# Kernel tuning notes

Hardware: AMD Instinct MI355X
Metric: run time of the kernel (lower is better)

Reference implementation:

```python
import jax, jax.numpy as jnp
import numpy as np

N = 50000      # nodes
E = 800000     # graph edges
NNZ = 800000   # hypergraph incidence entries
M = 10000      # hyperedges
IN, HID, OUT = 128, 64, 64


def setup_inputs() -> dict:
    key = jax.random.key(0)
    ks = jax.random.split(key, 12)
    x = jax.random.normal(ks[0], (N, IN), dtype=jnp.float32)
    edge_index = jax.random.randint(ks[1], (2, E), 0, N)
    node_idx = jax.random.randint(ks[2], (NNZ,), 0, N)
    he_idx = jax.random.randint(ks[3], (NNZ,), 0, M)
    hyperedge_index = jnp.stack([node_idx, he_idx])
    w = lambda k, fi, fo: jax.random.normal(k, (fi, fo), jnp.float32) / np.sqrt(fi)
    return {
        "x": x,
        "edge_index": edge_index,
        "hyperedge_index": hyperedge_index,
        "gcn1_w": w(ks[4], IN, HID), "gcn1_b": jnp.zeros((HID,), jnp.float32),
        "gcn2_w": w(ks[5], HID, OUT), "gcn2_b": jnp.zeros((OUT,), jnp.float32),
        "hyper1_w": w(ks[6], IN, HID), "hyper1_b": jnp.zeros((HID,), jnp.float32),
        "hyper2_w": w(ks[7], HID, OUT), "hyper2_b": jnp.zeros((OUT,), jnp.float32),
        "fusion_gate": jnp.zeros((1,), jnp.float32),
    }


def gcn_conv(x, edge_index, w, b):
    # PyG GCNConv: add self-loops, symmetric normalization, then aggregate.
    xw = x @ w
    loops = jnp.arange(N)
    row = jnp.concatenate([edge_index[0], loops])  # source j
    col = jnp.concatenate([edge_index[1], loops])  # target i
    deg = jax.ops.segment_sum(jnp.ones_like(col, dtype=xw.dtype), col, num_segments=N)
    dis = jnp.where(deg > 0, jax.lax.rsqrt(jnp.maximum(deg, 1e-12)), 0.0)
    norm = dis[row] * dis[col]
    out = jax.ops.segment_sum(norm[:, None] * xw[row], col, num_segments=N)
    return out + b


def hyper_conv(x, hyperedge_index, w, b):
    # PyG HypergraphConv (no attention, unit hyperedge weights):
    # out = D^{-1} H B^{-1} H^T (X W) + b
    xw = x @ w
    node_idx, he_idx = hyperedge_index[0], hyperedge_index[1]
    ones = jnp.ones((hyperedge_index.shape[1],), dtype=xw.dtype)
    D = jax.ops.segment_sum(ones, node_idx, num_segments=N)   # node degree
    B = jax.ops.segment_sum(ones, he_idx, num_segments=M)     # hyperedge degree
    Dinv = jnp.where(D > 0, 1.0 / jnp.maximum(D, 1e-12), 0.0)
    Binv = jnp.where(B > 0, 1.0 / jnp.maximum(B, 1e-12), 0.0)
    edge_feat = Binv[:, None] * jax.ops.segment_sum(xw[node_idx], he_idx, num_segments=M)
    out = Dinv[:, None] * jax.ops.segment_sum(edge_feat[he_idx], node_idx, num_segments=N)
    return out + b


def reference(x, edge_index, hyperedge_index,
              gcn1_w, gcn1_b, gcn2_w, gcn2_b,
              hyper1_w, hyper1_b, hyper2_w, hyper2_b,
              fusion_gate):
    # dropout is identity in eval mode (deterministic reference)
    x_s = gcn_conv(x, edge_index, gcn1_w, gcn1_b)
    x_s = jax.nn.elu(x_s)
    x_s = gcn_conv(x_s, edge_index, gcn2_w, gcn2_b)
    x_d = hyper_conv(x, hyperedge_index, hyper1_w, hyper1_b)
    x_d = jax.nn.elu(x_d)
    x_d = hyper_conv(x_d, hyperedge_index, hyper2_w, hyper2_b)
    alpha = jax.nn.sigmoid(fusion_gate)  # shape (1,), broadcasts
    z = alpha * x_s + (1.0 - alpha) * x_d
    return (z, x_s, x_d)
```

## Files before the change

kernel.cpp:

```cpp
#include <hip/hip_runtime.h>
#include <hip/hip_bf16.h>

#define N_NODES 50000
#define N_EDGES 800000
#define NNZ_H   800000
#define M_HE    10000
#define F_IN    128
#define F_HID   64

#define SH_E 7
#define NB_E ((N_NODES + 127) >> 7)
#define SH_H 5
#define NB_H ((M_HE + 31) >> 5)
#define SH_N 7
#define NB_N ((N_NODES + 127) >> 7)
#define TILE 4096
#define GB   ((N_EDGES + TILE - 1) / TILE)
#define NBMAX 400
#define KPBMAX 128
#define GG  782
#define GWN 12500

static __device__ __forceinline__ float bflo(unsigned v) { return __uint_as_float(v << 16); }
static __device__ __forceinline__ float bfhi(unsigned v) { return __uint_as_float(v & 0xFFFF0000u); }

__global__ void k_hist_all(const int* __restrict__ e_col, const int* __restrict__ h_idx,
                           const int* __restrict__ n_idx,
                           int* __restrict__ bcntE, int* __restrict__ bcntH, int* __restrict__ bcntN) {
    __shared__ int hE[NB_E], hH[NB_H], hN[NB_N];
    for (int i = threadIdx.x; i < NB_E; i += 256) hE[i] = 0;
    for (int i = threadIdx.x; i < NB_H; i += 256) hH[i] = 0;
    for (int i = threadIdx.x; i < NB_N; i += 256) hN[i] = 0;
    __syncthreads();
    int stride = gridDim.x * 256;
    for (int i = blockIdx.x * 256 + threadIdx.x; i < N_EDGES; i += stride) {
        atomicAdd(&hE[e_col[i] >> SH_E], 1);
        atomicAdd(&hH[h_idx[i] >> SH_H], 1);
        atomicAdd(&hN[n_idx[i] >> SH_N], 1);
    }
    __syncthreads();
    for (int i = threadIdx.x; i < NB_E; i += 256) if (hE[i]) atomicAdd(&bcntE[i], hE[i]);
    for (int i = threadIdx.x; i < NB_H; i += 256) if (hH[i]) atomicAdd(&bcntH[i], hH[i]);
    for (int i = threadIdx.x; i < NB_N; i += 256) if (hN[i]) atomicAdd(&bcntN[i], hN[i]);
}

__device__ void scan_block(const int* __restrict__ in, int* __restrict__ out, int n) {
    __shared__ int s[1024];
    int t = threadIdx.x;
    int chunk = (n + 1023) >> 10;
    int b = t * chunk;
    int e = min(b + chunk, n);
    int sum = 0;
    for (int i = b; i < e; ++i) sum += in[i];
    s[t] = sum;
    __syncthreads();
    for (int d = 1; d < 1024; d <<= 1) {
        int v = (t >= d) ? s[t - d] : 0;
        __syncthreads();
        s[t] += v;
        __syncthreads();
    }
    int run = (t > 0) ? s[t - 1] : 0;
    for (int i = b; i < e; ++i) { int v = in[i]; out[i] = run; run += v; }
}
__global__ void k_scan_buckets(const int* __restrict__ bcntE, int* __restrict__ boffE,
                               const int* __restrict__ bcntH, int* __restrict__ boffH,
                               const int* __restrict__ bcntN, int* __restrict__ boffN) {
    if (blockIdx.x == 0)      scan_block(bcntE, boffE, NB_E);
    else if (blockIdx.x == 1) scan_block(bcntH, boffH, NB_H);
    else                      scan_block(bcntN, boffN, NB_N);
}

__device__ void chunk_scatter(const int* __restrict__ keys, const int* __restrict__ vals,
                              int n, int sh, int nb,
                              const int* __restrict__ boff, int* __restrict__ bcur,
                              int* __restrict__ bk, int blk) {
    __shared__ int h[NBMAX], loc[NBMAX], base[NBMAX], hc[NBMAX];
    __shared__ int buf[TILE];
    __shared__ unsigned short bkt[TILE];
    int t0 = blk * TILE;
    int tend = min(t0 + TILE, n);
    int cnt = tend - t0;
    for (int b = threadIdx.x; b < nb; b += 256) { h[b] = 0; hc[b] = 0; }
    __syncthreads();
    for (int i = t0 + threadIdx.x; i < tend; i += 256)
        atomicAdd(&h[keys[i] >> sh], 1);
    __syncthreads();
    if (threadIdx.x == 0) {
        int run = 0;
        for (int b = 0; b < nb; ++b) { loc[b] = run; run += h[b]; }
    }
    __syncthreads();
    for (int b = threadIdx.x; b < nb; b += 256)
        base[b] = boff[b] + atomicAdd(&bcur[b], h[b]);
    __syncthreads();
    for (int i = t0 + threadIdx.x; i < tend; i += 256) {
        int k = keys[i];
        int b = k >> sh;
        int r = loc[b] + atomicAdd(&hc[b], 1);
        buf[r] = ((k - (b << sh)) << 16) | vals[i];
        bkt[r] = (unsigned short)b;
    }
    __syncthreads();
    for (int j = threadIdx.x; j < cnt; j += 256) {
        int b = bkt[j];
        bk[base[b] + (j - loc[b])] = buf[j];
    }
}
__global__ void k_chunk_all(const int* __restrict__ e_row, const int* __restrict__ e_col,
                            const int* __restrict__ n_idx, const int* __restrict__ h_idx,
                            const int* __restrict__ boffE, int* __restrict__ bcurE, int* __restrict__ bkE,
                            const int* __restrict__ boffH, int* __restrict__ bcurH, int* __restrict__ bkH,
                            const int* __restrict__ boffN, int* __restrict__ bcurN, int* __restrict__ bkN) {
    int gb = blockIdx.x;
    if (gb < GB)            chunk_scatter(e_col, e_row, N_EDGES, SH_E, NB_E, boffE, bcurE, bkE, gb);
    else if (gb < 2 * GB)   chunk_scatter(h_idx, n_idx, NNZ_H,  SH_H, NB_H, boffH, bcurH, bkH, gb - GB);
    else                    chunk_scatter(n_idx, h_idx, NNZ_H,  SH_N, NB_N, boffN, bcurN, bkN, gb - 2 * GB);
}

__global__ void k_fin_all(const int* __restrict__ bkE, const int* __restrict__ boffE,
                          int* __restrict__ srtE, int* __restrict__ offE,
                          const int* __restrict__ bkH, const int* __restrict__ boffH,
                          int* __restrict__ srtH, int* __restrict__ offH,
                          const int* __restrict__ bkN, const int* __restrict__ boffN,
                          int* __restrict__ srtN, int* __restrict__ offN) {
    __shared__ int koff[KPBMAX];
    __shared__ int kcur[KPBMAX];
    __shared__ int tsum[256];
    int b = blockIdx.x;
    const int* bk; const int* boff; int* srt; int* off;
    int nb, sh, nkeys, total;
    if (b < NB_E) {
        bk = bkE; boff = boffE; srt = srtE; off = offE;
        nb = NB_E; sh = SH_E; nkeys = N_NODES; total = N_EDGES;
    } else if (b < NB_E + NB_H) {
        b -= NB_E;
        bk = bkH; boff = boffH; srt = srtH; off = offH;
        nb = NB_H; sh = SH_H; nkeys = M_HE; total = NNZ_H;
    } else {
        b -= NB_E + NB_H;
        bk = bkN; boff = boffN; srt = srtN; off = offN;
        nb = NB_N; sh = SH_N; nkeys = N_NODES; total = NNZ_H;
    }
    int kpb = 1 << sh;
    int k0 = b << sh;
    int beg = boff[b];
    int end = (b + 1 < nb) ? boff[b + 1] : total;
    int t = threadIdx.x;
    if (t < kpb) { koff[t] = 0; kcur[t] = 0; }
    __syncthreads();
    for (int i = beg + t; i < end; i += 256)
        atomicAdd(&koff[((unsigned)bk[i]) >> 16], 1);
    __syncthreads();
    int v = (t < kpb) ? koff[t] : 0;
    tsum[t] = v;
    __syncthreads();
    for (int d = 1; d < 256; d <<= 1) {
        int u = (t >= d) ? tsum[t - d] : 0;
        __syncthreads();
        tsum[t] += u;
        __syncthreads();
    }
    if (t < kpb) koff[t] = tsum[t] - v;
    __syncthreads();
    if (t < kpb && (k0 + t) < nkeys) off[k0 + t] = beg + koff[t];
    if (b == nb - 1 && t == 0) off[nkeys] = total;
    for (int i = beg + t; i < end; i += 256) {
        int p = bk[i];
        int lk = ((unsigned)p) >> 16;
        int pos = beg + koff[lk] + atomicAdd(&kcur[lk], 1);
        srt[pos] = p & 0xFFFF;
    }
}

template<int K, bool SCALE>
__device__ __forceinline__ void gemm_body(const float* __restrict__ xin, const float* __restrict__ w,
                                          const int* __restrict__ offE, __hip_bfloat16* __restrict__ out,
                                          int blk, float* __restrict__ wl, float* __restrict__ xs) {
    int tid = threadIdx.x;
    int wv = tid >> 6, lane = tid & 63;
    int cg = lane & 15;
    int rg = lane >> 4;
    int rl = wv * 16 + rg * 4;
    int r0 = blk * 64;
    float acc[4][4] = {};
    for (int k0 = 0; k0 < K; k0 += 64) {
        {
            const float4* wsrc = (const float4*)(w + k0 * 64);
            float4* wdst = (float4*)wl;
            for (int j = tid; j < 1024; j += 256) wdst[j] = wsrc[j];
        }
        for (int p = tid; p < 1024; p += 256) {
            int r = p >> 4, c4 = p & 15;
            int row = min(r0 + r, N_NODES - 1);
            float4 vv = *(const float4*)(xin + (size_t)row * K + k0 + 4 * c4);
            *(float4*)&xs[r * 68 + 4 * c4] = vv;
        }
        __syncthreads();
#pragma unroll 4
        for (int kk = 0; kk < 64; ++kk) {
            float4 wf = *(const float4*)&wl[kk * 64 + cg * 4];
            float x0 = xs[(rl + 0) * 68 + kk];
            float x1 = xs[(rl + 1) * 68 + kk];
            float x2 = xs[(rl + 2) * 68 + kk];
            float x3 = xs[(rl + 3) * 68 + kk];
            acc[0][0] += x0 * wf.x; acc[0][1] += x0 * wf.y; acc[0][2] += x0 * wf.z; acc[0][3] += x0 * wf.w;
            acc[1][0] += x1 * wf.x; acc[1][1] += x1 * wf.y; acc[1][2] += x1 * wf.z; acc[1][3] += x1 * wf.w;
            acc[2][0] += x2 * wf.x; acc[2][1] += x2 * wf.y; acc[2][2] += x2 * wf.z; acc[2][3] += x2 * wf.w;
            acc[3][0] += x3 * wf.x; acc[3][1] += x3 * wf.y; acc[3][2] += x3 * wf.z; acc[3][3] += x3 * wf.w;
        }
        __syncthreads();
    }
#pragma unroll
    for (int i = 0; i < 4; ++i) {
        int row = r0 + rl + i;
        if (row < N_NODES) {
            float s = 1.0f;
            if (SCALE) {
                float deg = (float)(offE[row + 1] - offE[row]);
                s = rsqrtf(deg + 1.0f);
            }
            __hip_bfloat16 hv[4];
            hv[0] = __float2bfloat16(acc[i][0] * s);
            hv[1] = __float2bfloat16(acc[i][1] * s);
            hv[2] = __float2bfloat16(acc[i][2] * s);
            hv[3] = __float2bfloat16(acc[i][3] * s);
            *(ushort4*)&out[(size_t)row * 64 + cg * 4] = *(ushort4*)hv;
        }
    }
}

template<int K>
__global__ void k_gemm_dual(const float* __restrict__ in1, const float* __restrict__ w1,
                            const int* __restrict__ offE, __hip_bfloat16* __restrict__ out1,
                            const float* __restrict__ in2, const float* __restrict__ w2,
                            __hip_bfloat16* __restrict__ out2) {
    __shared__ float wl[64 * 64];
    __shared__ float xs[64 * 68];
    if (blockIdx.x < GG) gemm_body<K, true>(in1, w1, offE, out1, blockIdx.x, wl, xs);
    else                 gemm_body<K, false>(in2, w2, nullptr, out2, blockIdx.x - GG, wl, xs);
}

template<bool ELU>
__device__ __forceinline__ void gcn_gather_body(const int* __restrict__ off, const int* __restrict__ srcs,
                                                const __hip_bfloat16* __restrict__ xw,
                                                const float* __restrict__ b,
                                                float* __restrict__ out, int blk) {
    int tid = threadIdx.x;
    int wv = tid >> 6, lane = tid & 63;
    int h = lane >> 5, l = lane & 31;
    int wid = blk * 4 + wv;
    if (wid >= N_NODES) return;
    int beg = off[wid];
    int cnt = off[wid + 1] - beg;
    const unsigned* xwu = (const unsigned*)xw;
    float ax0 = 0, ay0 = 0, ax1 = 0, ay1 = 0, ax2 = 0, ay2 = 0, ax3 = 0, ay3 = 0;
    int k = h;
    for (; k + 6 < cnt; k += 8) {
        int s0 = srcs[beg + k];
        int s1 = srcs[beg + k + 2];
        int s2 = srcs[beg + k + 4];
        int s3 = srcs[beg + k + 6];
        unsigned v0 = xwu[(size_t)s0 * 32 + l];
        unsigned v1 = xwu[(size_t)s1 * 32 + l];
        unsigned v2 = xwu[(size_t)s2 * 32 + l];
        unsigned v3 = xwu[(size_t)s3 * 32 + l];
        ax0 += bflo(v0); ay0 += bfhi(v0);
        ax1 += bflo(v1); ay1 += bfhi(v1);
        ax2 += bflo(v2); ay2 += bfhi(v2);
        ax3 += bflo(v3); ay3 += bfhi(v3);
    }
    for (; k < cnt; k += 2) {
        unsigned v = xwu[(size_t)srcs[beg + k] * 32 + l];
        ax0 += bflo(v); ay0 += bfhi(v);
    }
    float tx = (ax0 + ax1) + (ax2 + ax3);
    float ty = (ay0 + ay1) + (ay2 + ay3);
    tx += __shfl_xor(tx, 32);
    ty += __shfl_xor(ty, 32);
    unsigned sv = xwu[(size_t)wid * 32 + l];
    float di = rsqrtf((float)cnt + 1.0f);
    float vx = di * (tx + bflo(sv)) + b[2 * l];
    float vy = di * (ty + bfhi(sv)) + b[2 * l + 1];
    if (ELU) {
        vx = (vx > 0.0f) ? vx : expm1f(vx);
        vy = (vy > 0.0f) ? vy : expm1f(vy);
    }
    if (h == 0) *(float2*)(out + (size_t)wid * 64 + 2 * l) = make_float2(vx, vy);
}

__device__ __forceinline__ void he_gather_body(const int* __restrict__ off, const int* __restrict__ nodes,
                                               const __hip_bfloat16* __restrict__ xw,
                                               float* __restrict__ C, int he, float2 (*red)[32]) {
    int tid = threadIdx.x;
    int wv = tid >> 6, lane = tid & 63;
    int h = lane >> 5, l = lane & 31;
    int beg = off[he], end = off[he + 1];
    int cnt = end - beg;
    int per = (cnt + 3) >> 2;
    int b0 = beg + wv * per;
    int e0 = min(b0 + per, end);
    int c2 = e0 - b0;
    const unsigned* xwu = (const unsigned*)xw;
    float ax0 = 0, ay0 = 0, ax1 = 0, ay1 = 0;
    int k = h;
    for (; k + 2 < c2; k += 4) {
        unsigned v0 = xwu[(size_t)nodes[b0 + k] * 32 + l];
        unsigned v1 = xwu[(size_t)nodes[b0 + k + 2] * 32 + l];
        ax0 += bflo(v0); ay0 += bfhi(v0);
        ax1 += bflo(v1); ay1 += bfhi(v1);
    }
    for (; k < c2; k += 2) {
        unsigned v = xwu[(size_t)nodes[b0 + k] * 32 + l];
        ax0 += bflo(v); ay0 += bfhi(v);
    }
    float tx = ax0 + ax1;
    float ty = ay0 + ay1;
    tx += __shfl_xor(tx, 32);
    ty += __shfl_xor(ty, 32);
    if (h == 0) red[wv][l] = make_float2(tx, ty);
    __syncthreads();
    if (tid < 32) {
        float2 r0 = red[0][tid], r1 = red[1][tid], r2 = red[2][tid], r3 = red[3][tid];
        float binv = (cnt > 0) ? 1.0f / (float)cnt : 0.0f;
        float2 o = make_float2((r0.x + r1.x + r2.x + r3.x) * binv,
                               (r0.y + r1.y + r2.y + r3.y) * binv);
        *(float2*)(C + (size_t)he * 64 + 2 * tid) = o;
    }
}

template<bool ELU>
__global__ __launch_bounds__(256, 8)
void k_gather_dual(const int* __restrict__ offE, const int* __restrict__ srtE,
                   const __hip_bfloat16* __restrict__ A, const float* __restrict__ gb,
                   float* __restrict__ aggOut,
                   const int* __restrict__ offH, const int* __restrict__ srtH,
                   const __hip_bfloat16* __restrict__ B, float* __restrict__ C) {
    __shared__ float2 red[4][32];
    if (blockIdx.x < GWN) gcn_gather_body<ELU>(offE, srtE, A, gb, aggOut, blockIdx.x);
    else                  he_gather_body(offH, srtH, B, C, blockIdx.x - GWN, red);
}

template<bool ELU, bool FUSE>
__global__ __launch_bounds__(256, 8)
void k_node_gather(const int* __restrict__ off, const int* __restrict__ hes,
                   const float* __restrict__ C, const float* __restrict__ b,
                   float* __restrict__ out,
                   const float* __restrict__ xs, const float* __restrict__ gate,
                   float* __restrict__ z) {
    int tid = threadIdx.x;
    int wv = tid >> 6, lane = tid & 63;
    int h = lane >> 5, l = lane & 31;
    int wid = blockIdx.x * 4 + wv;
    if (wid >= N_NODES) return;
    int beg = off[wid];
    int cnt = off[wid + 1] - beg;
    float ax0 = 0, ay0 = 0, ax1 = 0, ay1 = 0, ax2 = 0, ay2 = 0, ax3 = 0, ay3 = 0;
    int k = h;
    for (; k + 6 < cnt; k += 8) {
        float2 c0 = *(const float2*)(C + (size_t)hes[beg + k] * 64 + 2 * l);
        float2 c1 = *(const float2*)(C + (size_t)hes[beg + k + 2] * 64 + 2 * l);
        float2 c2 = *(const float2*)(C + (size_t)hes[beg + k + 4] * 64 + 2 * l);
        float2 c3 = *(const float2*)(C + (size_t)hes[beg + k + 6] * 64 + 2 * l);
        ax0 += c0.x; ay0 += c0.y;
        ax1 += c1.x; ay1 += c1.y;
        ax2 += c2.x; ay2 += c2.y;
        ax3 += c3.x; ay3 += c3.y;
    }
    for (; k < cnt; k += 2) {
        float2 c = *(const float2*)(C + (size_t)hes[beg + k] * 64 + 2 * l);
        ax0 += c.x; ay0 += c.y;
    }
    float tx = (ax0 + ax1) + (ax2 + ax3);
    float ty = (ay0 + ay1) + (ay2 + ay3);
    tx += __shfl_xor(tx, 32);
    ty += __shfl_xor(ty, 32);
    float dinv = (cnt > 0) ? 1.0f / (float)cnt : 0.0f;
    float vx = dinv * tx + b[2 * l];
    float vy = dinv * ty + b[2 * l + 1];
    if (ELU) {
        vx = (vx > 0.0f) ? vx : expm1f(vx);
        vy = (vy > 0.0f) ? vy : expm1f(vy);
    }
    if (h == 0) {
        size_t idx = (size_t)wid * 64 + 2 * l;
        *(float2*)(out + idx) = make_float2(vx, vy);
        if (FUSE) {
            float a = 1.0f / (1.0f + expf(-gate[0]));
            float2 s = *(const float2*)(xs + idx);
            *(float2*)(z + idx) = make_float2(a * s.x + (1.0f - a) * vx,
                                              a * s.y + (1.0f - a) * vy);
        }
    }
}

extern "C" void kernel_launch(void* const* d_in, const int* in_sizes, int n_in,
                              void* d_out, int out_size, void* d_ws, size_t ws_size,
                              hipStream_t stream) {
    const float* x      = (const float*)d_in[0];
    const int*   ei     = (const int*)d_in[1];
    const int*   hei    = (const int*)d_in[2];
    const float* gcn1_w = (const float*)d_in[3];
    const float* gcn1_b = (const float*)d_in[4];
    const float* gcn2_w = (const float*)d_in[5];
    const float* gcn2_b = (const float*)d_in[6];
    const float* hyp1_w = (const float*)d_in[7];
    const float* hyp1_b = (const float*)d_in[8];
    const float* hyp2_w = (const float*)d_in[9];
    const float* hyp2_b = (const float*)d_in[10];
    const float* gate   = (const float*)d_in[11];
    float* out = (float*)d_out;

    const int* e_row = ei;
    const int* e_col = ei + N_EDGES;
    const int* n_idx = hei;
    const int* h_idx = hei + NNZ_H;

    const size_t NV = (size_t)N_NODES * 64;
    float* z_out  = out;
    float* xs_out = out + NV;
    float* xd_out = out + 2 * NV;

    char* base = (char*)d_ws;
    __hip_bfloat16* Abf = (__hip_bfloat16*)base;
    __hip_bfloat16* Bbf = (__hip_bfloat16*)(base + NV * 2);
    float* AGG1 = (float*)(base + NV * 4);
    float* AGG2 = (float*)(base + NV * 8);
    float* C    = (float*)(base + NV * 12);
    int* srtE = (int*)(C + (size_t)M_HE * 64);
    int* srtH = srtE + N_EDGES;
    int* srtN = srtH + NNZ_H;
    int* offE = srtN + NNZ_H;
    int* offH = offE + (N_NODES + 1);
    int* offN = offH + (M_HE + 1);
    int* bcntE = offN + (N_NODES + 1);
    int* bcntH = bcntE + NB_E;
    int* bcntN = bcntH + NB_H;
    int* bcurE = bcntN + NB_N;
    int* bcurH = bcurE + NB_E;
    int* bcurN = bcurH + NB_H;
    int* boffE = bcurN + NB_N;
    int* boffH = boffE + NB_E;
    int* boffN = boffH + NB_H;
    const size_t zero_ints = 2 * (size_t)(NB_E + NB_H + NB_N);
    int* bkE = (int*)Abf;
    int* bkH = (int*)Bbf;
    int* bkN = (int*)AGG1;

    const int BLK = 256;

    hipMemsetAsync(bcntE, 0, zero_ints * sizeof(int), stream);
    k_hist_all<<<256, BLK, 0, stream>>>(e_col, h_idx, n_idx, bcntE, bcntH, bcntN);
    k_scan_buckets<<<3, 1024, 0, stream>>>(bcntE, boffE, bcntH, boffH, bcntN, boffN);
    k_chunk_all<<<3 * GB, BLK, 0, stream>>>(e_row, e_col, n_idx, h_idx,
                                            boffE, bcurE, bkE,
                                            boffH, bcurH, bkH,
                                            boffN, bcurN, bkN);
    k_fin_all<<<NB_E + NB_H + NB_N, BLK, 0, stream>>>(bkE, boffE, srtE, offE,
                                                      bkH, boffH, srtH, offH,
                                                      bkN, boffN, srtN, offN);

    k_gemm_dual<F_IN><<<2 * GG, BLK, 0, stream>>>(x, gcn1_w, offE, Abf, x, hyp1_w, Bbf);
    k_gather_dual<true><<<GWN + M_HE, BLK, 0, stream>>>(offE, srtE, Abf, gcn1_b, AGG1,
                                                        offH, srtH, Bbf, C);
    k_node_gather<true, false><<<GWN, BLK, 0, stream>>>(offN, srtN, C, hyp1_b, AGG2,
                                                        nullptr, nullptr, nullptr);
    k_gemm_dual<F_HID><<<2 * GG, BLK, 0, stream>>>(AGG1, gcn2_w, offE, Abf, AGG2, hyp2_w, Bbf);
    k_gather_dual<false><<<GWN + M_HE, BLK, 0, stream>>>(offE, srtE, Abf, gcn2_b, xs_out,
                                                         offH, srtH, Bbf, C);
    k_node_gather<false, true><<<GWN, BLK, 0, stream>>>(offN, srtN, C, hyp2_b, xd_out,
                                                        xs_out, gate, z_out);

    (void)in_sizes; (void)n_in; (void)out_size; (void)ws_size;
}
```

Before: 279.8 us.

## Fold bucket scan into scatter kernels, vectorize histogram, deepen gather unrolling

```diff
diff --git a/kernel.cpp b/kernel.cpp
--- a/kernel.cpp
+++ b/kernel.cpp
@@ -32,11 +32,20 @@
     for (int i = threadIdx.x; i < NB_H; i += 256) hH[i] = 0;
     for (int i = threadIdx.x; i < NB_N; i += 256) hN[i] = 0;
     __syncthreads();
+    const int2* ec2 = (const int2*)e_col;
+    const int2* hi2 = (const int2*)h_idx;
+    const int2* ni2 = (const int2*)n_idx;
     int stride = gridDim.x * 256;
-    for (int i = blockIdx.x * 256 + threadIdx.x; i < N_EDGES; i += stride) {
-        atomicAdd(&hE[e_col[i] >> SH_E], 1);
-        atomicAdd(&hH[h_idx[i] >> SH_H], 1);
-        atomicAdd(&hN[n_idx[i] >> SH_N], 1);
+    for (int i = blockIdx.x * 256 + threadIdx.x; i < N_EDGES / 2; i += stride) {
+        int2 e = ec2[i];
+        atomicAdd(&hE[e.x >> SH_E], 1);
+        atomicAdd(&hE[e.y >> SH_E], 1);
+        int2 hh = hi2[i];
+        atomicAdd(&hH[hh.x >> SH_H], 1);
+        atomicAdd(&hH[hh.y >> SH_H], 1);
+        int2 nn = ni2[i];
+        atomicAdd(&hN[nn.x >> SH_N], 1);
+        atomicAdd(&hN[nn.y >> SH_N], 1);
     }
     __syncthreads();
     for (int i = threadIdx.x; i < NB_E; i += 256) if (hE[i]) atomicAdd(&bcntE[i], hE[i]);
@@ -44,40 +53,34 @@
     for (int i = threadIdx.x; i < NB_N; i += 256) if (hN[i]) atomicAdd(&bcntN[i], hN[i]);
 }
 
-__device__ void scan_block(const int* __restrict__ in, int* __restrict__ out, int n) {
-    __shared__ int s[1024];
+__device__ void scan_to_lds(const int* __restrict__ in, int* __restrict__ soff, int nb,
+                            int* __restrict__ tsum) {
     int t = threadIdx.x;
-    int chunk = (n + 1023) >> 10;
-    int b = t * chunk;
-    int e = min(b + chunk, n);
-    int sum = 0;
-    for (int i = b; i < e; ++i) sum += in[i];
-    s[t] = sum;
-    __syncthreads();
-    for (int d = 1; d < 1024; d <<= 1) {
-        int v = (t >= d) ? s[t - d] : 0;
+    int v0 = (2 * t < nb) ? in[2 * t] : 0;
+    int v1 = (2 * t + 1 < nb) ? in[2 * t + 1] : 0;
+    tsum[t] = v0 + v1;
+    __syncthreads();
+    for (int d = 1; d < 256; d <<= 1) {
+        int u = (t >= d) ? tsum[t - d] : 0;
         __syncthreads();
-        s[t] += v;
+        tsum[t] += u;
         __syncthreads();
     }
-    int run = (t > 0) ? s[t - 1] : 0;
-    for (int i = b; i < e; ++i) { int v = in[i]; out[i] = run; run += v; }
-}
-__global__ void k_scan_buckets(const int* __restrict__ bcntE, int* __restrict__ boffE,
-                               const int* __restrict__ bcntH, int* __restrict__ boffH,
-                               const int* __restrict__ bcntN, int* __restrict__ boffN) {
-    if (blockIdx.x == 0)      scan_block(bcntE, boffE, NB_E);
-    else if (blockIdx.x == 1) scan_block(bcntH, boffH, NB_H);
-    else                      scan_block(bcntN, boffN, NB_N);
+    int run = (t > 0) ? tsum[t - 1] : 0;
+    if (2 * t < nb) soff[2 * t] = run;
+    if (2 * t + 1 < nb) soff[2 * t + 1] = run + v0;
+    __syncthreads();
 }
 
 __device__ void chunk_scatter(const int* __restrict__ keys, const int* __restrict__ vals,
                               int n, int sh, int nb,
-                              const int* __restrict__ boff, int* __restrict__ bcur,
+                              const int* __restrict__ bcnt, int* __restrict__ bcur,
                               int* __restrict__ bk, int blk) {
-    __shared__ int h[NBMAX], loc[NBMAX], base[NBMAX], hc[NBMAX];
+    __shared__ int h[NBMAX], loc[NBMAX], base[NBMAX], hc[NBMAX], soff[NBMAX];
+    __shared__ int tsum[256];
     __shared__ int buf[TILE];
     __shared__ unsigned short bkt[TILE];
+    scan_to_lds(bcnt, soff, nb, tsum);
     int t0 = blk * TILE;
     int tend = min(t0 + TILE, n);
     int cnt = tend - t0;
@@ -92,7 +95,7 @@
     }
     __syncthreads();
     for (int b = threadIdx.x; b < nb; b += 256)
-        base[b] = boff[b] + atomicAdd(&bcur[b], h[b]);
+        base[b] = soff[b] + atomicAdd(&bcur[b], h[b]);
     __syncthreads();
     for (int i = t0 + threadIdx.x; i < tend; i += 256) {
         int k = keys[i];
@@ -109,43 +112,45 @@
 }
 __global__ void k_chunk_all(const int* __restrict__ e_row, const int* __restrict__ e_col,
                             const int* __restrict__ n_idx, const int* __restrict__ h_idx,
-                            const int* __restrict__ boffE, int* __restrict__ bcurE, int* __restrict__ bkE,
-                            const int* __restrict__ boffH, int* __restrict__ bcurH, int* __restrict__ bkH,
-                            const int* __restrict__ boffN, int* __restrict__ bcurN, int* __restrict__ bkN) {
+                            const int* __restrict__ bcntE, int* __restrict__ bcurE, int* __restrict__ bkE,
+                            const int* __restrict__ bcntH, int* __restrict__ bcurH, int* __restrict__ bkH,
+                            const int* __restrict__ bcntN, int* __restrict__ bcurN, int* __restrict__ bkN) {
     int gb = blockIdx.x;
-    if (gb < GB)            chunk_scatter(e_col, e_row, N_EDGES, SH_E, NB_E, boffE, bcurE, bkE, gb);
-    else if (gb < 2 * GB)   chunk_scatter(h_idx, n_idx, NNZ_H,  SH_H, NB_H, boffH, bcurH, bkH, gb - GB);
-    else                    chunk_scatter(n_idx, h_idx, NNZ_H,  SH_N, NB_N, boffN, bcurN, bkN, gb - 2 * GB);
-}
-
-__global__ void k_fin_all(const int* __restrict__ bkE, const int* __restrict__ boffE,
+    if (gb < GB)            chunk_scatter(e_col, e_row, N_EDGES, SH_E, NB_E, bcntE, bcurE, bkE, gb);
+    else if (gb < 2 * GB)   chunk_scatter(h_idx, n_idx, NNZ_H,  SH_H, NB_H, bcntH, bcurH, bkH, gb - GB);
+    else                    chunk_scatter(n_idx, h_idx, NNZ_H,  SH_N, NB_N, bcntN, bcurN, bkN, gb - 2 * GB);
+}
+
+__global__ void k_fin_all(const int* __restrict__ bkE, const int* __restrict__ bcntE,
                           int* __restrict__ srtE, int* __restrict__ offE,
-                          const int* __restrict__ bkH, const int* __restrict__ boffH,
+                          const int* __restrict__ bkH, const int* __restrict__ bcntH,
                           int* __restrict__ srtH, int* __restrict__ offH,
-                          const int* __restrict__ bkN, const int* __restrict__ boffN,
+                          const int* __restrict__ bkN, const int* __restrict__ bcntN,
                           int* __restrict__ srtN, int* __restrict__ offN) {
     __shared__ int koff[KPBMAX];
     __shared__ int kcur[KPBMAX];
     __shared__ int tsum[256];
+    __shared__ int soff[NBMAX];
     int b = blockIdx.x;
-    const int* bk; const int* boff; int* srt; int* off;
+    const int* bk; const int* bcnt; int* srt; int* off;
     int nb, sh, nkeys, total;
     if (b < NB_E) {
-        bk = bkE; boff = boffE; srt = srtE; off = offE;
+        bk = bkE; bcnt = bcntE; srt = srtE; off = offE;
         nb = NB_E; sh = SH_E; nkeys = N_NODES; total = N_EDGES;
     } else if (b < NB_E + NB_H) {
         b -= NB_E;
-        bk = bkH; boff = boffH; srt = srtH; off = offH;
+        bk = bkH; bcnt = bcntH; srt = srtH; off = offH;
         nb = NB_H; sh = SH_H; nkeys = M_HE; total = NNZ_H;
     } else {
         b -= NB_E + NB_H;
-        bk = bkN; boff = boffN; srt = srtN; off = offN;
+        bk = bkN; bcnt = bcntN; srt = srtN; off = offN;
         nb = NB_N; sh = SH_N; nkeys = N_NODES; total = NNZ_H;
     }
+    scan_to_lds(bcnt, soff, nb, tsum);
     int kpb = 1 << sh;
     int k0 = b << sh;
-    int beg = boff[b];
-    int end = (b + 1 < nb) ? boff[b + 1] : total;
+    int beg = soff[b];
+    int end = (b + 1 < nb) ? soff[b + 1] : total;
     int t = threadIdx.x;
     if (t < kpb) { koff[t] = 0; kcur[t] = 0; }
     __syncthreads();
@@ -256,11 +261,31 @@
     const unsigned* xwu = (const unsigned*)xw;
     float ax0 = 0, ay0 = 0, ax1 = 0, ay1 = 0, ax2 = 0, ay2 = 0, ax3 = 0, ay3 = 0;
     int k = h;
+    for (; k + 14 < cnt; k += 16) {
+        int s0 = srcs[beg + k],      s1 = srcs[beg + k + 2];
+        int s2 = srcs[beg + k + 4],  s3 = srcs[beg + k + 6];
+        int s4 = srcs[beg + k + 8],  s5 = srcs[beg + k + 10];
+        int s6 = srcs[beg + k + 12], s7 = srcs[beg + k + 14];
+        unsigned v0 = xwu[(size_t)s0 * 32 + l];
+        unsigned v1 = xwu[(size_t)s1 * 32 + l];
+        unsigned v2 = xwu[(size_t)s2 * 32 + l];
+        unsigned v3 = xwu[(size_t)s3 * 32 + l];
+        unsigned v4 = xwu[(size_t)s4 * 32 + l];
+        unsigned v5 = xwu[(size_t)s5 * 32 + l];
+        unsigned v6 = xwu[(size_t)s6 * 32 + l];
+        unsigned v7 = xwu[(size_t)s7 * 32 + l];
+        ax0 += bflo(v0); ay0 += bfhi(v0);
+        ax1 += bflo(v1); ay1 += bfhi(v1);
+        ax2 += bflo(v2); ay2 += bfhi(v2);
+        ax3 += bflo(v3); ay3 += bfhi(v3);
+        ax0 += bflo(v4); ay0 += bfhi(v4);
+        ax1 += bflo(v5); ay1 += bfhi(v5);
+        ax2 += bflo(v6); ay2 += bfhi(v6);
+        ax3 += bflo(v7); ay3 += bfhi(v7);
+    }
     for (; k + 6 < cnt; k += 8) {
-        int s0 = srcs[beg + k];
-        int s1 = srcs[beg + k + 2];
-        int s2 = srcs[beg + k + 4];
-        int s3 = srcs[beg + k + 6];
+        int s0 = srcs[beg + k],     s1 = srcs[beg + k + 2];
+        int s2 = srcs[beg + k + 4], s3 = srcs[beg + k + 6];
         unsigned v0 = xwu[(size_t)s0 * 32 + l];
         unsigned v1 = xwu[(size_t)s1 * 32 + l];
         unsigned v2 = xwu[(size_t)s2 * 32 + l];
@@ -302,20 +327,48 @@
     int e0 = min(b0 + per, end);
     int c2 = e0 - b0;
     const unsigned* xwu = (const unsigned*)xw;
-    float ax0 = 0, ay0 = 0, ax1 = 0, ay1 = 0;
+    float ax0 = 0, ay0 = 0, ax1 = 0, ay1 = 0, ax2 = 0, ay2 = 0, ax3 = 0, ay3 = 0;
     int k = h;
-    for (; k + 2 < c2; k += 4) {
-        unsigned v0 = xwu[(size_t)nodes[b0 + k] * 32 + l];
-        unsigned v1 = xwu[(size_t)nodes[b0 + k + 2] * 32 + l];
+    for (; k + 14 < c2; k += 16) {
+        int s0 = nodes[b0 + k],      s1 = nodes[b0 + k + 2];
+        int s2 = nodes[b0 + k + 4],  s3 = nodes[b0 + k + 6];
+        int s4 = nodes[b0 + k + 8],  s5 = nodes[b0 + k + 10];
+        int s6 = nodes[b0 + k + 12], s7 = nodes[b0 + k + 14];
+        unsigned v0 = xwu[(size_t)s0 * 32 + l];
+        unsigned v1 = xwu[(size_t)s1 * 32 + l];
+        unsigned v2 = xwu[(size_t)s2 * 32 + l];
+        unsigned v3 = xwu[(size_t)s3 * 32 + l];
+        unsigned v4 = xwu[(size_t)s4 * 32 + l];
+        unsigned v5 = xwu[(size_t)s5 * 32 + l];
+        unsigned v6 = xwu[(size_t)s6 * 32 + l];
+        unsigned v7 = xwu[(size_t)s7 * 32 + l];
         ax0 += bflo(v0); ay0 += bfhi(v0);
         ax1 += bflo(v1); ay1 += bfhi(v1);
+        ax2 += bflo(v2); ay2 += bfhi(v2);
+        ax3 += bflo(v3); ay3 += bfhi(v3);
+        ax0 += bflo(v4); ay0 += bfhi(v4);
+        ax1 += bflo(v5); ay1 += bfhi(v5);
+        ax2 += bflo(v6); ay2 += bfhi(v6);
+        ax3 += bflo(v7); ay3 += bfhi(v7);
+    }
+    for (; k + 6 < c2; k += 8) {
+        int s0 = nodes[b0 + k],     s1 = nodes[b0 + k + 2];
+        int s2 = nodes[b0 + k + 4], s3 = nodes[b0 + k + 6];
+        unsigned v0 = xwu[(size_t)s0 * 32 + l];
+        unsigned v1 = xwu[(size_t)s1 * 32 + l];
+        unsigned v2 = xwu[(size_t)s2 * 32 + l];
+        unsigned v3 = xwu[(size_t)s3 * 32 + l];
+        ax0 += bflo(v0); ay0 += bfhi(v0);
+        ax1 += bflo(v1); ay1 += bfhi(v1);
+        ax2 += bflo(v2); ay2 += bfhi(v2);
+        ax3 += bflo(v3); ay3 += bfhi(v3);
     }
     for (; k < c2; k += 2) {
         unsigned v = xwu[(size_t)nodes[b0 + k] * 32 + l];
         ax0 += bflo(v); ay0 += bfhi(v);
     }
-    float tx = ax0 + ax1;
-    float ty = ay0 + ay1;
+    float tx = (ax0 + ax1) + (ax2 + ax3);
+    float ty = (ay0 + ay1) + (ay2 + ay3);
     tx += __shfl_xor(tx, 32);
     ty += __shfl_xor(ty, 32);
     if (h == 0) red[wv][l] = make_float2(tx, ty);
@@ -330,7 +383,7 @@
 }
 
 template<bool ELU>
-__global__ __launch_bounds__(256, 8)
+__global__ __launch_bounds__(256, 6)
 void k_gather_dual(const int* __restrict__ offE, const int* __restrict__ srtE,
                    const __hip_bfloat16* __restrict__ A, const float* __restrict__ gb,
                    float* __restrict__ aggOut,
@@ -439,9 +492,6 @@
     int* bcurE = bcntN + NB_N;
     int* bcurH = bcurE + NB_E;
     int* bcurN = bcurH + NB_H;
-    int* boffE = bcurN + NB_N;
-    int* boffH = boffE + NB_E;
-    int* boffN = boffH + NB_H;
     const size_t zero_ints = 2 * (size_t)(NB_E + NB_H + NB_N);
     int* bkE = (int*)Abf;
     int* bkH = (int*)Bbf;
@@ -451,14 +501,13 @@
 
     hipMemsetAsync(bcntE, 0, zero_ints * sizeof(int), stream);
     k_hist_all<<<256, BLK, 0, stream>>>(e_col, h_idx, n_idx, bcntE, bcntH, bcntN);
-    k_scan_buckets<<<3, 1024, 0, stream>>>(bcntE, boffE, bcntH, boffH, bcntN, boffN);
     k_chunk_all<<<3 * GB, BLK, 0, stream>>>(e_row, e_col, n_idx, h_idx,
-                                            boffE, bcurE, bkE,
-                                            boffH, bcurH, bkH,
-                                            boffN, bcurN, bkN);
-    k_fin_all<<<NB_E + NB_H + NB_N, BLK, 0, stream>>>(bkE, boffE, srtE, offE,
-                                                      bkH, boffH, srtH, offH,
-                                                      bkN, boffN, srtN, offN);
+                                            bcntE, bcurE, bkE,
+                                            bcntH, bcurH, bkH,
+                                            bcntN, bcurN, bkN);
+    k_fin_all<<<NB_E + NB_H + NB_N, BLK, 0, stream>>>(bkE, bcntE, srtE, offE,
+                                                      bkH, bcntH, srtH, offH,
+                                                      bkN, bcntN, srtN, offN);
 
     k_gemm_dual<F_IN><<<2 * GG, BLK, 0, stream>>>(x, gcn1_w, offE, Abf, x, hyp1_w, Bbf);
     k_gather_dual<true><<<GWN + M_HE, BLK, 0, stream>>>(offE, srtE, Abf, gcn1_b, AGG1,
```

Result: faster. 259.9 us (-7.1%).
